# Kernel tuning notes

Measured on AMD Instinct MI355X. Metric: run time of the kernel, lower is better.

The kernel has to match this reference:

```python
import jax, jax.numpy as jnp
import numpy as np

B, S, H = 2, 2048, 4096
NH, NKV, HD = 32, 8, 128
EPS = 1e-6


def _rope_tables(seq_len, head_dim, base=10000.0):
    inv = 1.0 / (base ** (np.arange(0, head_dim, 2, dtype=np.float32) / head_dim))
    t = np.arange(seq_len, dtype=np.float32)
    freqs = np.outer(t, inv)                       # [S, HD/2]
    emb = np.concatenate([freqs, freqs], axis=-1)  # [S, HD] (HF rotate_half layout)
    return jnp.asarray(np.cos(emb)), jnp.asarray(np.sin(emb))


def setup_inputs() -> dict:
    key = jax.random.key(0)
    ks = jax.random.split(key, 6)
    x = jax.random.normal(ks[0], (B, S, H), dtype=jnp.float32)
    wq = jax.random.normal(ks[1], (NH * HD, H), dtype=jnp.float32) * 0.02
    wk = jax.random.normal(ks[2], (NKV * HD, H), dtype=jnp.float32) * 0.02
    wv = jax.random.normal(ks[3], (NKV * HD, H), dtype=jnp.float32) * 0.02
    wo = jax.random.normal(ks[4], (H, NH * HD), dtype=jnp.float32) * 0.02
    cos1, sin1 = _rope_tables(S, HD)
    cos = jnp.broadcast_to(cos1[None], (B, S, HD))
    sin = jnp.broadcast_to(sin1[None], (B, S, HD))
    return {
        "x": x, "cos": cos, "sin": sin,
        "wq": wq, "wk": wk, "wv": wv, "wo": wo,
        "q_norm_w": jnp.ones((HD,), jnp.float32),
        "k_norm_w": jnp.ones((HD,), jnp.float32),
    }


def _rms_norm(x, w):
    # fp32 RMSNorm over last dim, scaled by per-head-dim weight
    xf = x.astype(jnp.float32)
    n = xf * jax.lax.rsqrt(jnp.mean(xf * xf, axis=-1, keepdims=True) + EPS)
    return n.astype(x.dtype) * w


def _rotate_half(x):
    x1, x2 = jnp.split(x, 2, axis=-1)
    return jnp.concatenate([-x2, x1], axis=-1)


def reference(x, cos, sin, wq, wk, wv, wo, q_norm_w, k_norm_w):
    bs, seqlen, _ = x.shape
    # projections (nn.Linear: y = x @ W^T)
    xq = (x @ wq.T).reshape(bs, seqlen, NH, HD)
    xk = (x @ wk.T).reshape(bs, seqlen, NKV, HD)
    xv = (x @ wv.T).reshape(bs, seqlen, NKV, HD)
    # per-head RMSNorm before RoPE
    xq = _rms_norm(xq, q_norm_w)
    xk = _rms_norm(xk, k_norm_w)
    # [b, h, s, d]
    xq = xq.transpose(0, 2, 1, 3)
    xk = xk.transpose(0, 2, 1, 3)
    xv = xv.transpose(0, 2, 1, 3)
    # RoPE, cos/sin broadcast over heads
    c = cos[:, None, :, :]
    s = sin[:, None, :, :]
    xq = xq * c + _rotate_half(xq) * s
    xk = xk * c + _rotate_half(xk) * s
    # GQA: repeat kv heads
    rep = NH // NKV
    if rep > 1:
        xk = jnp.repeat(xk, rep, axis=1)
        xv = jnp.repeat(xv, rep, axis=1)
    # causal SDPA
    scale = 1.0 / jnp.sqrt(jnp.float32(HD))
    scores = jnp.einsum("bhqd,bhkd->bhqk", xq, xk) * scale
    mask = jnp.tril(jnp.ones((seqlen, seqlen), bool))
    scores = jnp.where(mask, scores, jnp.finfo(scores.dtype).min)
    probs = jax.nn.softmax(scores, axis=-1)
    out = jnp.einsum("bhqk,bhkd->bhqd", probs, xv)
    out = out.transpose(0, 2, 1, 3).reshape(bs, seqlen, NH * HD)
    return out @ wo.T
```

## Files before the change

kernel.cpp:

```cpp
#include <hip/hip_runtime.h>
#include <hip/hip_bf16.h>

#define NB  2
#define SS  2048
#define HH  4096
#define NH  32
#define NKV 8
#define HD  128
#define MR  (NB*SS)

typedef __bf16 bf16x8 __attribute__((ext_vector_type(8)));
typedef float  f32x4  __attribute__((ext_vector_type(4)));
typedef float  f32x16 __attribute__((ext_vector_type(16)));
using bf16 = __hip_bfloat16;

__device__ __forceinline__ f32x4 mfma16(bf16x8 a, bf16x8 b, f32x4 c) {
  return __builtin_amdgcn_mfma_f32_16x16x32_bf16(a, b, c, 0, 0, 0);
}
__device__ __forceinline__ f32x16 mfma32(bf16x8 a, bf16x8 b, f32x16 c) {
  return __builtin_amdgcn_mfma_f32_32x32x16_bf16(a, b, c, 0, 0, 0);
}
__device__ __forceinline__ unsigned cvtpk(float lo, float hi) {
  unsigned r; asm("v_cvt_pk_bf16_f32 %0, %1, %2" : "=v"(r) : "v"(lo), "v"(hi));
  return r;
}
__device__ __forceinline__ void swap32(unsigned &a, unsigned &b) {
  asm volatile("v_permlane32_swap_b32 %0, %1" : "+v"(a), "+v"(b));
}
__device__ __forceinline__ float fexp2(float x) {
  float r; asm("v_exp_f32 %0, %1" : "=v"(r) : "v"(x)); return r;
}

typedef const __attribute__((address_space(1))) void gv_t;
typedef __attribute__((address_space(3))) void lv_t;
__device__ __forceinline__ void gload16(const void* g, void* l) {
  __builtin_amdgcn_global_load_lds((gv_t*)g, (lv_t*)l, 16, 0, 0);
}
#define CFENCE asm volatile("" ::: "memory")

__global__ void f2b5(const float* __restrict__ s0, const float* __restrict__ s1,
                     const float* __restrict__ s2, const float* __restrict__ s3,
                     const float* __restrict__ s4,
                     bf16* __restrict__ d0, bf16* __restrict__ d1,
                     bf16* __restrict__ d2, bf16* __restrict__ d3,
                     bf16* __restrict__ d4)
{
  const unsigned c0 = 4194304u, c1 = 8388608u, c2 = 9437184u, c3 = 10485760u,
                 c4 = 14680064u;
  unsigned i = blockIdx.x*blockDim.x + threadIdx.x;
  unsigned stride = gridDim.x*blockDim.x;
  for (unsigned u = i; u < c4; u += stride) {
    const float* s; bf16* d; unsigned off;
    if (u < c0)      { s = s0; d = d0; off = u; }
    else if (u < c1) { s = s1; d = d1; off = u - c0; }
    else if (u < c2) { s = s2; d = d2; off = u - c1; }
    else if (u < c3) { s = s3; d = d3; off = u - c2; }
    else             { s = s4; d = d4; off = u - c3; }
    float4 v = *(const float4*)(s + (size_t)off*4);
    __hip_bfloat16 b0 = __float2bfloat16(v.x);
    __hip_bfloat16 b1 = __float2bfloat16(v.y);
    __hip_bfloat16 b2 = __float2bfloat16(v.z);
    __hip_bfloat16 b3 = __float2bfloat16(v.w);
    ushort4 o;
    o.x = *reinterpret_cast<unsigned short*>(&b0);
    o.y = *reinterpret_cast<unsigned short*>(&b1);
    o.z = *reinterpret_cast<unsigned short*>(&b2);
    o.w = *reinterpret_cast<unsigned short*>(&b3);
    *(ushort4*)((unsigned short*)d + (size_t)off*4) = o;
  }
}

template<typename OutT>
__global__ __launch_bounds__(512, 2) void gemm256(
    const bf16* __restrict__ A, const bf16* __restrict__ Bt, OutT* __restrict__ C,
    int M, int N, int K, int tilesX)
{
  __shared__ bf16 lds[2*2*2*8192];

  const int bid = blockIdx.x;
  const int cpx = gridDim.x >> 3;
  const int wg  = (bid & 7)*cpx + (bid >> 3);
  const int m0 = (wg / tilesX) * 256, n0 = (wg % tilesX) * 256;

  const int tid = threadIdx.x;
  const int l = tid & 63;
  const int l15 = l & 15, lhi = l >> 4;
  const int wid = tid >> 6;
  const int wr = wid >> 2, wc = wid & 3;

  const int srow = tid >> 2;
  const int sps  = tid & 3;
  const int sls  = (sps - (srow >> 1)) & 3;
  const bf16* ga0 = A  + (size_t)(m0 + srow)*K       + sls*8;
  const bf16* ga1 = A  + (size_t)(m0 + srow + 128)*K + sls*8;
  const bf16* gb0 = Bt + (size_t)(n0 + srow)*K       + sls*8;
  const bf16* gb1 = Bt + (size_t)(n0 + srow + 128)*K + sls*8;
  const int ldst = tid*8;

#define REG(buf, mat, ks) (&lds[(((buf)*2 + (mat))*2 + (ks))*8192])
#define STG_A(buf, ks, kofs) do {                                 \
    gload16(ga0 + (kofs), REG(buf,0,ks) + ldst);                  \
    gload16(ga1 + (kofs), REG(buf,0,ks) + ldst + 4096);           \
  } while (0)
#define STG_B(buf, ks, kofs) do {                                 \
    gload16(gb0 + (kofs), REG(buf,1,ks) + ldst);                  \
    gload16(gb1 + (kofs), REG(buf,1,ks) + ldst + 4096);           \
  } while (0)

  f32x4 acc[8][4];
  #pragma unroll
  for (int fm = 0; fm < 8; ++fm)
    #pragma unroll
    for (int fn = 0; fn < 4; ++fn)
      #pragma unroll
      for (int e = 0; e < 4; ++e) acc[fm][fn][e] = 0.f;

  const int arow = wr*128 + l15;
  const int brow = wc*64  + l15;
  const int psl  = (lhi + (l15 >> 1)) & 3;

  bf16x8 bv[4];

#define PHASE(PB, KS, FMH, RB, STG, WN) do {                               \
    const bf16* Ar_ = REG(PB, 0, KS);                                      \
    const bf16* Br_ = REG(PB, 1, KS);                                      \
    bf16x8 af[4];                                                          \
    for (int fm = 0; fm < 4; ++fm)                                         \
      af[fm] = *(const bf16x8*)(Ar_ + (arow + (FMH)*64 + fm*16)*32 + psl*8); \
    if (RB) {                                                              \
      for (int fn = 0; fn < 4; ++fn)                                       \
        bv[fn] = *(const bf16x8*)(Br_ + (brow + fn*16)*32 + psl*8);        \
    }                                                                      \
    STG;                                                                   \
    CFENCE;                                                                \
    __builtin_amdgcn_s_barrier();                                          \
    __builtin_amdgcn_s_setprio(1);                                         \
    for (int fm = 0; fm < 4; ++fm)                                         \
      for (int fn = 0; fn < 4; ++fn)                                       \
        acc[(FMH)*4 + fm][fn] = mfma16(af[fm], bv[fn], acc[(FMH)*4 + fm][fn]); \
    __builtin_amdgcn_s_setprio(0);                                         \
    if ((WN) == 6)      asm volatile("s_waitcnt vmcnt(6)" ::: "memory");   \
    else if ((WN) == 0) asm volatile("s_waitcnt vmcnt(0)" ::: "memory");   \
    __builtin_amdgcn_s_barrier();                                          \
    CFENCE;                                                                \
  } while (0)

  const int nt = K >> 6;

  STG_A(0, 0, 0);  STG_B(0, 0, 0);  STG_A(0, 1, 32);  STG_B(0, 1, 32);
  STG_A(1, 0, 64); STG_B(1, 0, 64); STG_B(1, 1, 96);
  asm volatile("s_waitcnt vmcnt(6)" ::: "memory");
  __builtin_amdgcn_s_barrier();
  CFENCE;

  for (int i = 0; i < (nt >> 1) - 1; ++i) {
    const int t  = i << 1;
    const int k1 = ((t + 1) << 6) + 32;
    const int k2 = (t + 2) << 6;
    const int k3 = (t + 3) << 6;
    PHASE(0, 0, 0, true,  STG_A(1, 1, k1),      -1);
    PHASE(0, 0, 1, false, STG_B(0, 0, k2),      -1);
    PHASE(0, 1, 0, true,  STG_A(0, 0, k2),      -1);
    PHASE(0, 1, 1, false, STG_B(0, 1, k2 + 32),  6);
    PHASE(1, 0, 0, true,  STG_A(0, 1, k2 + 32), -1);
    PHASE(1, 0, 1, false, STG_B(1, 0, k3),      -1);
    PHASE(1, 1, 0, true,  STG_A(1, 0, k3),      -1);
    PHASE(1, 1, 1, false, STG_B(1, 1, k3 + 32),  6);
  }
  {
    const int k1 = ((nt - 1) << 6) + 32;
    PHASE(0, 0, 0, true,  STG_A(1, 1, k1), -1);
    PHASE(0, 0, 1, false, (void)0,         -1);
    PHASE(0, 1, 0, true,  (void)0,         -1);
    PHASE(0, 1, 1, false, (void)0,          0);
    PHASE(1, 0, 0, true,  (void)0,         -1);
    PHASE(1, 0, 1, false, (void)0,         -1);
    PHASE(1, 1, 0, true,  (void)0,         -1);
    PHASE(1, 1, 1, false, (void)0,         -1);
  }
#undef PHASE
#undef STG_A
#undef STG_B
#undef REG

  #pragma unroll
  for (int fm = 0; fm < 8; ++fm) {
    const int crow = m0 + wr*128 + fm*16 + lhi*4;
    #pragma unroll
    for (int fn = 0; fn < 4; ++fn) {
      const int ccol = n0 + wc*64 + fn*16 + l15;
      #pragma unroll
      for (int j = 0; j < 4; ++j) {
        if constexpr (sizeof(OutT) == 2)
          C[(size_t)(crow + j)*N + ccol] = __float2bfloat16(acc[fm][fn][j]);
        else
          C[(size_t)(crow + j)*N + ccol] = acc[fm][fn][j];
      }
    }
  }
}

__global__ __launch_bounds__(256) void normrope(
    const bf16* __restrict__ src, bf16* __restrict__ dst,
    const float* __restrict__ cosb, const float* __restrict__ sinb,
    const float* __restrict__ w, int nh, float scale, int rowstride, int coloff)
{
  const int wid = threadIdx.x >> 6, lane = threadIdx.x & 63;
  const int row = blockIdx.x*4 + wid;
  const int m = row / nh, h = row % nh;
  const int b = m / SS, s = m % SS;
  const bf16* sp = src + (size_t)m*rowstride + coloff + h*HD;
  float v1 = __bfloat162float(sp[lane]);
  float v2 = __bfloat162float(sp[lane + 64]);
  float ss = v1*v1 + v2*v2;
  #pragma unroll
  for (int msk = 1; msk < 64; msk <<= 1) ss += __shfl_xor(ss, msk);
  float r = rsqrtf(ss*(1.f/128.f) + 1e-6f) * scale;
  float n1 = v1*r*w[lane], n2 = v2*r*w[lane + 64];
  const float* cp  = cosb + (size_t)m*HD;
  const float* sip = sinb + (size_t)m*HD;
  float o1 = n1*cp[lane]      - n2*sip[lane];
  float o2 = n2*cp[lane + 64] + n1*sip[lane + 64];
  bf16* dp = dst + ((size_t)(b*nh + h)*SS + s)*HD;
  dp[lane]      = __float2bfloat16(o1);
  dp[lane + 64] = __float2bfloat16(o2);
}

__global__ __launch_bounds__(256) void vtrans(const bf16* __restrict__ v0,
                                              bf16* __restrict__ vt,
                                              int rowstride, int coloff)
{
  __shared__ bf16 tile[64][65];
  const int s0 = blockIdx.x*64, d0 = blockIdx.y*64, bkv = blockIdx.z;
  const int bb = bkv >> 3, kv = bkv & 7;
  const int c = threadIdx.x & 63, rbase = threadIdx.x >> 6;
  #pragma unroll
  for (int r = 0; r < 64; r += 4) {
    int sl = r + rbase;
    tile[sl][c] = v0[(size_t)(bb*SS + s0 + sl)*rowstride + coloff + kv*HD + d0 + c];
  }
  __syncthreads();
  #pragma unroll
  for (int r = 0; r < 64; r += 4) {
    int dl = r + rbase;
    vt[((size_t)bkv*HD + d0 + dl)*SS + s0 + c] = tile[c][dl];
  }
}

__global__ __launch_bounds__(512, 2) void attn_fwd(
    const bf16* __restrict__ qr, const bf16* __restrict__ kr,
    const bf16* __restrict__ vt, bf16* __restrict__ ao)
{
  __shared__ __align__(16) char smem[65536];

  const int L = blockIdx.x;
  const int orig = (L & 7)*64 + (L >> 3);
  const int bh = orig >> 3, j = orig & 7;
  const int b = bh >> 5, h = bh & 31, kvh = h >> 2;

  const int tid = threadIdx.x;
  const int wid = tid >> 6, lane = tid & 63;
  const int l31 = lane & 31, hi = lane >> 5;
  const unsigned hi16 = hi << 4;
  const unsigned swz = (lane & 7) << 4;

  const int qw0 = (wid < 4) ? (j*128 + wid*32) : ((15 - j)*128 + (wid - 4)*32);
  const int NT = 32 - 2*j;
  const int qlane = qw0 + l31;

  const bf16* Qp = qr + ((size_t)(b*NH + h)*SS + qlane)*HD;
  const bf16* Kp = kr + (size_t)(b*NKV + kvh)*SS*HD;
  const bf16* Vp = vt + (size_t)(b*NKV + kvh)*HD*SS;

  const int krA = tid >> 4;
  const int ksA = tid & 15;
  const int vrA = tid >> 3;
  const int vsA = tid & 7;
  const int kswz = (ksA ^ (krA & 7))*8;
  const int vswz = (vsA ^ (vrA & 7))*8;

#define STAGE_ATTN(buf, kvbase) do {                                        \
    char* kb = smem + (buf)*32768;                                          \
    char* vb = kb + 16384;                                                  \
    gload16(Kp + (size_t)(krA + (kvbase))*HD + kswz,      kb + tid*16);     \
    gload16(Kp + (size_t)(krA + 32 + (kvbase))*HD + kswz, kb + 8192 + tid*16); \
    gload16(Vp + (size_t)vrA*SS + (kvbase) + vswz,        vb + tid*16);     \
    gload16(Vp + (size_t)(vrA + 64)*SS + (kvbase) + vswz, vb + 8192 + tid*16); \
  } while (0)

  STAGE_ATTN(0, 0);
  bf16x8 qf[8];
  #pragma unroll
  for (int kd = 0; kd < 8; ++kd)
    qf[kd] = *(const bf16x8*)(Qp + kd*16 + hi*8);
  asm volatile("s_waitcnt vmcnt(0)" ::: "memory");
  __builtin_amdgcn_s_barrier();
  CFENCE;

  f32x16 o0, o1, o2, o3;
  #pragma unroll
  for (int r = 0; r < 16; ++r) { o0[r] = 0.f; o1[r] = 0.f; o2[r] = 0.f; o3[r] = 0.f; }
  float mrow = -1e30f, lrow = 0.f;

  for (int t = 0; t < NT; ++t) {
    const int p = t & 1;
    const char* KsB = smem + p*32768;
    const char* VsB = KsB + 16384;
    if (t + 1 < NT) STAGE_ATTN(p ^ 1, (t + 1)*64);
    const int kv0 = t*64;

    if (kv0 <= qw0 + 31) {
      f32x16 s0, s1;
      #pragma unroll
      for (int r = 0; r < 16; ++r) { s0[r] = 0.f; s1[r] = 0.f; }
      #pragma unroll
      for (int kd = 0; kd < 8; ++kd) {
        bf16x8 k0f = *(const bf16x8*)(KsB + l31*256        + (((unsigned)(kd*32) + hi16) ^ swz));
        bf16x8 k1f = *(const bf16x8*)(KsB + (32 + l31)*256 + (((unsigned)(kd*32) + hi16) ^ swz));
        s0 = mfma32(k0f, qf[kd], s0);
        s1 = mfma32(k1f, qf[kd], s1);
      }
      if (kv0 + 63 > qw0) {
        #pragma unroll
        for (int r = 0; r < 16; ++r) {
          const int off = (r & 3) + 8*(r >> 2) + 4*hi;
          if (kv0 + off > qlane)      s0[r] = -1e30f;
          if (kv0 + 32 + off > qlane) s1[r] = -1e30f;
        }
      }
      float tmax = s0[0];
      #pragma unroll
      for (int r = 1; r < 16; ++r) tmax = fmaxf(tmax, s0[r]);
      #pragma unroll
      for (int r = 0; r < 16; ++r) tmax = fmaxf(tmax, s1[r]);
      tmax = fmaxf(tmax, __shfl_xor(tmax, 32));
      if (!__all(tmax <= mrow + 8.f)) {
        float mnew = fmaxf(mrow, tmax);
        float alpha = fexp2(mrow - mnew);
        mrow = mnew;
        lrow *= alpha;
        #pragma unroll
        for (int r = 0; r < 16; ++r) {
          o0[r] *= alpha; o1[r] *= alpha; o2[r] *= alpha; o3[r] *= alpha;
        }
      }
      float tsum = 0.f;
      #pragma unroll
      for (int r = 0; r < 16; ++r) { s0[r] = fexp2(s0[r] - mrow); tsum += s0[r]; }
      #pragma unroll
      for (int r = 0; r < 16; ++r) { s1[r] = fexp2(s1[r] - mrow); tsum += s1[r]; }
      tsum += __shfl_xor(tsum, 32);
      lrow += tsum;

      #pragma unroll
      for (int ks = 0; ks < 4; ++ks) {
        const int bb0 = (ks & 1)*8;
        float p0,p1,p2,p3,p4,p5,p6,p7;
        if (ks < 2) { p0=s0[bb0+0];p1=s0[bb0+1];p2=s0[bb0+2];p3=s0[bb0+3];
                      p4=s0[bb0+4];p5=s0[bb0+5];p6=s0[bb0+6];p7=s0[bb0+7]; }
        else        { p0=s1[bb0+0];p1=s1[bb0+1];p2=s1[bb0+2];p3=s1[bb0+3];
                      p4=s1[bb0+4];p5=s1[bb0+5];p6=s1[bb0+6];p7=s1[bb0+7]; }
        unsigned c01 = cvtpk(p0,p1), c23 = cvtpk(p2,p3);
        unsigned c45 = cvtpk(p4,p5), c67 = cvtpk(p6,p7);
        unsigned w0 = c01, w2 = c45; swap32(w0, w2);
        unsigned w1 = c23, w3 = c67; swap32(w1, w3);
        union { unsigned u[4]; bf16x8 v; } pa;
        pa.u[0]=w0; pa.u[1]=w1; pa.u[2]=w2; pa.u[3]=w3;
        #pragma unroll
        for (int dt = 0; dt < 4; ++dt) {
          bf16x8 vf = *(const bf16x8*)(VsB + (dt*32 + l31)*128 +
                                       (((unsigned)(ks*32) + hi16) ^ swz));
          f32x16 &oo = (dt==0)?o0:(dt==1)?o1:(dt==2)?o2:o3;
          oo = mfma32(vf, pa.v, oo);
        }
      }
    }

    asm volatile("s_waitcnt vmcnt(0)" ::: "memory");
    __builtin_amdgcn_s_barrier();
    CFENCE;
  }
#undef STAGE_ATTN

  const float invl = 1.f / lrow;
  char* ow = smem + wid*4096;
  bf16* aop = ao + ((size_t)b*SS + qlane)*HH + h*HD;
  const unsigned eswz = (l31 & 7) << 4;
  #pragma unroll
  for (int half = 0; half < 2; ++half) {
    #pragma unroll
    for (int hh = 0; hh < 2; ++hh) {
      #pragma unroll
      for (int r = 0; r < 16; ++r) {
        const int dcol = hh*32 + (r & 3) + 8*(r >> 2) + 4*hi;
        float val = ((half*2+hh)==0 ? o0[r] : (half*2+hh)==1 ? o1[r]
                     : (half*2+hh)==2 ? o2[r] : o3[r]) * invl;
        *(bf16*)(ow + l31*128 + (((unsigned)(dcol*2)) ^ eswz)) = __float2bfloat16(val);
      }
    }
    #pragma unroll
    for (int m = 0; m < 4; ++m) {
      const int c0 = hi*32 + m*8;
      bf16x8 vv = *(const bf16x8*)(ow + l31*128 + (((unsigned)(c0*2)) ^ eswz));
      *(bf16x8*)(aop + half*64 + c0) = vv;
    }
  }
}

extern "C" void kernel_launch(void* const* d_in, const int* in_sizes, int n_in,
                              void* d_out, int out_size, void* d_ws, size_t ws_size,
                              hipStream_t stream)
{
  const float* x    = (const float*)d_in[0];
  const float* cosb = (const float*)d_in[1];
  const float* sinb = (const float*)d_in[2];
  const float* wq   = (const float*)d_in[3];
  const float* wk   = (const float*)d_in[4];
  const float* wv   = (const float*)d_in[5];
  const float* wo   = (const float*)d_in[6];
  const float* qnw  = (const float*)d_in[7];
  const float* knw  = (const float*)d_in[8];
  float* out = (float*)d_out;

  char* ws = (char*)d_ws;
  bf16* xb    = (bf16*)(ws);
  bf16* wqkvb = (bf16*)(ws +  33554432);
  bf16* wob   = (bf16*)(ws +  83886080);
  bf16* qkv0  = (bf16*)(ws + 117440512);
  bf16* qr    = (bf16*)(ws + 167772160);
  bf16* vt = xb;
  bf16* kr = (bf16*)(ws + 8388608);
  bf16* ao = qkv0;

  f2b5<<<2048, 256, 0, stream>>>(x, wq, wk, wv, wo,
                                 xb, wqkvb,
                                 wqkvb + (size_t)4096*4096,
                                 wqkvb + (size_t)5120*4096,
                                 wob);

  gemm256<bf16><<<384, 512, 0, stream>>>(xb, wqkvb, qkv0, MR, 6144, HH, 24);

  normrope<<<(MR*NH)/4,  256, 0, stream>>>(qkv0, qr, cosb, sinb, qnw, NH,
                                           0.08838834764831845f*1.44269504088896341f,
                                           6144, 0);
  normrope<<<(MR*NKV)/4, 256, 0, stream>>>(qkv0, kr, cosb, sinb, knw, NKV, 1.0f,
                                           6144, 4096);
  vtrans<<<dim3(32, 2, 16), 256, 0, stream>>>(qkv0, vt, 6144, 5120);

  attn_fwd<<<512, 512, 0, stream>>>(qr, kr, vt, ao);

  gemm256<float><<<256, 512, 0, stream>>>(ao, wob, out, MR, HH, HH, 16);
}
```

Measured before the change: 533.6 us.

## Split QKV projection into Q GEMM and smaller-tile KV GEMM

Replaces the single fused QKV GEMM, whose 384 large tiles run as 1.5 waves, with a Q GEMM of 256 tiles and a new 128x256-tile GEMM for K/V, also 256 tiles. Buffers and strides for normrope and vtrans are updated to the separate Q and KV outputs. The aim is to remove wave-quantization tail idle time. In exchange it adds a kernel launch, and the KV GEMM's smaller tiles mean less operand reuse.

Result: faster. 517.4 us (-3.0%).

```diff
diff --git a/kernel.cpp b/kernel.cpp
--- a/kernel.cpp
+++ b/kernel.cpp
@@ -200,6 +200,115 @@
   }
 }
 
+__global__ __launch_bounds__(512, 2) void gemm128n(
+    const bf16* __restrict__ A, const bf16* __restrict__ Bt, bf16* __restrict__ C,
+    int M, int N, int K, int tilesX)
+{
+  __shared__ bf16 lds[2*2*12288];
+
+  const int bid = blockIdx.x;
+  const int cpx = gridDim.x >> 3;
+  const int wg  = (bid & 7)*cpx + (bid >> 3);
+  const int m0 = (wg / tilesX) * 128, n0 = (wg % tilesX) * 256;
+
+  const int tid = threadIdx.x;
+  const int l = tid & 63;
+  const int l15 = l & 15, lhi = l >> 4;
+  const int wid = tid >> 6;
+  const int wr = wid >> 2, wc = wid & 3;
+
+  const int srow = tid >> 2;
+  const int sps  = tid & 3;
+  const int sls  = (sps - (srow >> 1)) & 3;
+  const bf16* gaA = A  + (size_t)(m0 + srow)*K       + sls*8;
+  const bf16* gb0 = Bt + (size_t)(n0 + srow)*K       + sls*8;
+  const bf16* gb1 = Bt + (size_t)(n0 + srow + 128)*K + sls*8;
+  const int ldst = tid*8;
+
+#define REGA(buf, ks) (&lds[((buf)*2 + (ks))*12288])
+#define REGB(buf, ks) (&lds[((buf)*2 + (ks))*12288 + 4096])
+#define STGKA(buf, ks, kofs) gload16(gaA + (kofs), REGA(buf,ks) + ldst)
+#define STGKB(buf, ks, kofs) do {                                 \
+    gload16(gb0 + (kofs), REGB(buf,ks) + ldst);                   \
+    gload16(gb1 + (kofs), REGB(buf,ks) + ldst + 4096);            \
+  } while (0)
+
+  f32x4 acc[4][4];
+  #pragma unroll
+  for (int fm = 0; fm < 4; ++fm)
+    #pragma unroll
+    for (int fn = 0; fn < 4; ++fn)
+      #pragma unroll
+      for (int e = 0; e < 4; ++e) acc[fm][fn][e] = 0.f;
+
+  const int arow = wr*64 + l15;
+  const int brow = wc*64 + l15;
+  const int psl  = (lhi + (l15 >> 1)) & 3;
+
+#define PHASEK(PB, KS, STG, WN) do {                                       \
+    const bf16* Ar_ = REGA(PB, KS);                                        \
+    const bf16* Br_ = REGB(PB, KS);                                        \
+    bf16x8 af[4], bv[4];                                                   \
+    for (int fm = 0; fm < 4; ++fm)                                         \
+      af[fm] = *(const bf16x8*)(Ar_ + (arow + fm*16)*32 + psl*8);          \
+    for (int fn = 0; fn < 4; ++fn)                                         \
+      bv[fn] = *(const bf16x8*)(Br_ + (brow + fn*16)*32 + psl*8);          \
+    STG;                                                                   \
+    CFENCE;                                                                \
+    __builtin_amdgcn_s_barrier();                                          \
+    __builtin_amdgcn_s_setprio(1);                                         \
+    for (int fm = 0; fm < 4; ++fm)                                         \
+      for (int fn = 0; fn < 4; ++fn)                                       \
+        acc[fm][fn] = mfma16(af[fm], bv[fn], acc[fm][fn]);                 \
+    __builtin_amdgcn_s_setprio(0);                                         \
+    if ((WN) == 6)      asm volatile("s_waitcnt vmcnt(6)" ::: "memory");   \
+    else if ((WN) == 0) asm volatile("s_waitcnt vmcnt(0)" ::: "memory");   \
+    __builtin_amdgcn_s_barrier();                                          \
+    CFENCE;                                                                \
+  } while (0)
+
+  const int nt = K >> 6;
+
+  STGKB(0, 0, 0);  STGKA(0, 0, 0);  STGKB(0, 1, 32);  STGKA(0, 1, 32);
+  STGKB(1, 0, 64); STGKA(1, 0, 64); STGKB(1, 1, 96);  STGKA(1, 1, 96);
+  asm volatile("s_waitcnt vmcnt(6)" ::: "memory");
+  __builtin_amdgcn_s_barrier();
+  CFENCE;
+
+  for (int i = 0; i < (nt >> 1) - 1; ++i) {
+    const int t  = i << 1;
+    const int k2 = (t + 2) << 6;
+    const int k3 = (t + 3) << 6;
+    PHASEK(0, 0, { STGKB(0, 0, k2);      STGKA(0, 0, k2);      }, -1);
+    PHASEK(0, 1, { STGKB(0, 1, k2 + 32); STGKA(0, 1, k2 + 32); },  6);
+    PHASEK(1, 0, { STGKB(1, 0, k3);      STGKA(1, 0, k3);      }, -1);
+    PHASEK(1, 1, { STGKB(1, 1, k3 + 32); STGKA(1, 1, k3 + 32); },  6);
+  }
+  {
+    PHASEK(0, 0, (void)0, -1);
+    PHASEK(0, 1, (void)0,  0);
+    PHASEK(1, 0, (void)0, -1);
+    PHASEK(1, 1, (void)0, -1);
+  }
+#undef PHASEK
+#undef STGKA
+#undef STGKB
+#undef REGA
+#undef REGB
+
+  #pragma unroll
+  for (int fm = 0; fm < 4; ++fm) {
+    const int crow = m0 + wr*64 + fm*16 + lhi*4;
+    #pragma unroll
+    for (int fn = 0; fn < 4; ++fn) {
+      const int ccol = n0 + wc*64 + fn*16 + l15;
+      #pragma unroll
+      for (int j = 0; j < 4; ++j)
+        C[(size_t)(crow + j)*N + ccol] = __float2bfloat16(acc[fm][fn][j]);
+    }
+  }
+}
+
 __global__ __launch_bounds__(256) void normrope(
     const bf16* __restrict__ src, bf16* __restrict__ dst,
     const float* __restrict__ cosb, const float* __restrict__ sinb,
@@ -426,11 +535,12 @@
   bf16* xb    = (bf16*)(ws);
   bf16* wqkvb = (bf16*)(ws +  33554432);
   bf16* wob   = (bf16*)(ws +  83886080);
-  bf16* qkv0  = (bf16*)(ws + 117440512);
+  bf16* q0    = (bf16*)(ws + 117440512);
+  bf16* kv0   = (bf16*)(ws + 150994944);
   bf16* qr    = (bf16*)(ws + 167772160);
   bf16* vt = xb;
   bf16* kr = (bf16*)(ws + 8388608);
-  bf16* ao = qkv0;
+  bf16* ao = q0;
 
   f2b5<<<2048, 256, 0, stream>>>(x, wq, wk, wv, wo,
                                  xb, wqkvb,
@@ -438,14 +548,16 @@
                                  wqkvb + (size_t)5120*4096,
                                  wob);
 
-  gemm256<bf16><<<384, 512, 0, stream>>>(xb, wqkvb, qkv0, MR, 6144, HH, 24);
-
-  normrope<<<(MR*NH)/4,  256, 0, stream>>>(qkv0, qr, cosb, sinb, qnw, NH,
+  gemm256<bf16><<<256, 512, 0, stream>>>(xb, wqkvb, q0, MR, 4096, HH, 16);
+  gemm128n<<<256, 512, 0, stream>>>(xb, wqkvb + (size_t)4096*4096, kv0,
+                                    MR, 2048, HH, 8);
+
+  normrope<<<(MR*NH)/4,  256, 0, stream>>>(q0, qr, cosb, sinb, qnw, NH,
                                            0.08838834764831845f*1.44269504088896341f,
-                                           6144, 0);
-  normrope<<<(MR*NKV)/4, 256, 0, stream>>>(qkv0, kr, cosb, sinb, knw, NKV, 1.0f,
-                                           6144, 4096);
-  vtrans<<<dim3(32, 2, 16), 256, 0, stream>>>(qkv0, vt, 6144, 5120);
+                                           4096, 0);
+  normrope<<<(MR*NKV)/4, 256, 0, stream>>>(kv0, kr, cosb, sinb, knw, NKV, 1.0f,
+                                           2048, 0);
+  vtrans<<<dim3(32, 2, 16), 256, 0, stream>>>(kv0, vt, 2048, 1024);
 
   attn_fwd<<<512, 512, 0, stream>>>(qr, kr, vt, ao);
 
```
